# Kernel tuning notes

Measured on AMD Instinct MI355X. Metric: run time of the kernel, lower is better.

The kernel has to match this reference:

```python
import jax, jax.numpy as jnp
import numpy as np

N = 8192      # nodes
E = 131072    # global edges
SDIM = 256    # scalar channels
VDIM = 64     # vector channels
EDIM = 128    # edge feature dim
L = 5         # num_layers
DIN = 2 * SDIM + EDIM + 4        # [s_src, s_tgt, e, d, a, |p_src|, |p_tgt|]
DOUT = SDIM + 2 * VDIM + 1 + EDIM  # [m_s, w_v1, w_v2, w_p, e_new]
HID = SDIM


def setup_inputs() -> dict:
    key = jax.random.key(0)
    ks = jax.random.split(key, 12)
    s = jax.random.normal(ks[0], (N, SDIM), jnp.float32)
    v = 0.1 * jax.random.normal(ks[1], (N, 3, VDIM), jnp.float32)
    p = 3.0 * jax.random.normal(ks[2], (N, 3), jnp.float32)
    e = jax.random.normal(ks[3], (E, EDIM), jnp.float32)
    edge_index = jax.random.randint(ks[4], (2, E), 0, N, dtype=jnp.int32)
    W1 = jax.random.normal(ks[5], (L, DIN, HID), jnp.float32) / np.sqrt(DIN)
    W2 = jax.random.normal(ks[6], (L, HID, DOUT), jnp.float32) / np.sqrt(HID)
    U1 = jax.random.normal(ks[7], (L, SDIM, SDIM), jnp.float32) / np.sqrt(SDIM)
    U2 = jax.random.normal(ks[8], (L, SDIM, SDIM), jnp.float32) / np.sqrt(SDIM)
    return {
        's': s, 'v': v, 'p': p, 'e': e, 'edge_index': edge_index,
        'ln_g': jnp.ones((L, SDIM), jnp.float32),
        'ln_b': jnp.zeros((L, SDIM), jnp.float32),
        'W1': W1, 'b1': jnp.zeros((L, HID), jnp.float32),
        'W2': W2, 'b2': jnp.zeros((L, DOUT), jnp.float32),
        'U1': U1, 'bU1': jnp.zeros((L, SDIM), jnp.float32),
        'U2': U2, 'bU2': jnp.zeros((L, SDIM), jnp.float32),
    }


def _edge_attrs(edge_index, pos):
    # Faithful to calculate_edge_attrs (sqrt=True, no ligand-pocket branch)
    src, tgt = edge_index[0], edge_index[1]
    r = pos[tgt] - pos[src]                                   # [E,3]
    a = jnp.sum(pos[tgt] * pos[src], axis=-1)                 # [E]
    d = jnp.sqrt(jnp.clip(jnp.sum(r * r, axis=-1), 1e-6, None))
    r_norm = r / (1.0 + d[:, None])
    return d, a, r_norm


def reference(s, v, p, e, edge_index, ln_g, ln_b, W1, b1, W2, b2, U1, bU1, U2, bU2):
    src, tgt = edge_index[0], edge_index[1]
    d, a, rn = _edge_attrs(edge_index, p)
    # in-degree counts for 'mean' vector/position aggregation
    cnt = jnp.clip(jax.ops.segment_sum(jnp.ones((E,), s.dtype), tgt, num_segments=N), 1.0)
    for i in range(L):
        # LayerNorm on scalar channels (vectors passed through)
        mu = jnp.mean(s, axis=-1, keepdims=True)
        var = jnp.mean((s - mu) ** 2, axis=-1, keepdims=True)
        s_ln = ln_g[i] * (s - mu) * jax.lax.rsqrt(var + 1e-5) + ln_b[i]
        pn = jnp.linalg.norm(p, axis=-1, keepdims=True)       # use_pos_norm features
        # gather-compute edge messages
        feat = jnp.concatenate(
            [s_ln[src], s_ln[tgt], e, d[:, None], a[:, None], pn[src], pn[tgt]], axis=-1)
        h = jax.nn.silu(feat @ W1[i] + b1[i])                 # [E,HID]
        out = h @ W2[i] + b2[i]                               # [E,DOUT]
        m_s = out[:, :SDIM]
        wv1 = out[:, SDIM:SDIM + VDIM]
        wv2 = out[:, SDIM + VDIM:SDIM + 2 * VDIM]
        wp = out[:, SDIM + 2 * VDIM:SDIM + 2 * VDIM + 1]
        e_new = out[:, SDIM + 2 * VDIM + 1:]
        has_v = 0.0 if i == 0 else 1.0                        # has_v_in = (i > 0)
        m_v = has_v * wv1[:, None, :] * v[src] + wv2[:, None, :] * rn[:, :, None]  # [E,3,VDIM]
        m_p = jnp.tanh(wp) * rn                               # [E,3]
        # scatter-aggregate (sum for scalars, mean for vectors/positions)
        s = s + jax.ops.segment_sum(m_s, tgt, num_segments=N)
        v = v + jax.ops.segment_sum(m_v, tgt, num_segments=N) / cnt[:, None, None]
        p = p + jax.ops.segment_sum(m_p, tgt, num_segments=N) / cnt[:, None]
        if i < L - 1:                                         # use_mlp_update = (i < num_layers - 1)
            s = s + jax.nn.silu(s @ U1[i] + bU1[i]) @ U2[i] + bU2[i]
        e = jax.nn.silu(e_new)
        # recompute_edge_attributes=True: redo gather/distance math on new positions
        d, a, rn = _edge_attrs(edge_index, p)
    return s, v, e, p
```

## Files before the change

### kernel.cpp

```cpp
#include <hip/hip_runtime.h>
#include <hip/hip_bf16.h>

namespace {

constexpr int NN   = 8192;
constexpr int NE   = 131072;
constexpr int SD   = 256;
constexpr int ED   = 128;
constexpr int NL   = 5;
constexpr int DINc = 644;
constexpr int KE   = 160;
constexpr int TE   = 5;
constexpr int T2   = 8;
constexpr int DOUTc= 513;
constexpr int HIDc = 256;

typedef __bf16 bf16x8 __attribute__((ext_vector_type(8)));
typedef float  f32x4  __attribute__((ext_vector_type(4)));

__device__ __forceinline__ float siluf(float x) { return x / (1.0f + __expf(-x)); }

__device__ __forceinline__ void gl_lds16(const void* gsrc, void* lds_uniform_base) {
  __builtin_amdgcn_global_load_lds(
      (const __attribute__((address_space(1))) unsigned int*)gsrc,
      (__attribute__((address_space(3))) unsigned int*)lds_uniform_base, 16, 0, 0);
}

__device__ __forceinline__ void wait_vm4() {
  asm volatile("s_waitcnt vmcnt(4)" ::: "memory");
  __builtin_amdgcn_sched_barrier(0);
}
__device__ __forceinline__ void wait_vm0() {
  asm volatile("s_waitcnt vmcnt(0)" ::: "memory");
  __builtin_amdgcn_sched_barrier(0);
}

__device__ __host__ __forceinline__ int swz(int kc) { return (kc * 5) & 7; }
__device__ __forceinline__ int apos(int kc, int row) { return kc * 64  + (row ^ swz(kc)); }
__device__ __forceinline__ int bpos(int kc, int n)   { return kc * 256 + (n   ^ swz(kc)); }

enum { SRC_BF16 = 1 };

struct GemmArgs {
  const __hip_bfloat16* Wt;
  const float* bias;
  const __hip_bfloat16* Abf;
  __hip_bfloat16* bf_out;
  const __hip_bfloat16* Wtb;
  const float* biasb;
  __hip_bfloat16* bf_outb;
  int dual;
};

__device__ __forceinline__ uint4 cvt8f(const float* p) {
  alignas(16) __hip_bfloat16 t8[8];
#pragma unroll
  for (int i = 0; i < 8; i++) t8[i] = __float2bfloat16(p[i]);
  return *(const uint4*)t8;
}

template<int KTOT, int BM>
__global__ __launch_bounds__(256) void gemm_k(GemmArgs g) {
  constexpr int T = KTOT / 32;
  constexpr int NC = KTOT / 8;
  constexpr int RPT = 256 / BM;
  constexpr int RMASK = RPT - 1;
  __shared__ alignas(16) unsigned short Apan[NC * BM * 8];
  __shared__ alignas(16) unsigned short Bsh[2][4 * 256 * 8];
  const int tid = threadIdx.x, lane = tid & 63, wave = tid >> 6;
  const int l16 = lane & 15, lhi = lane >> 4;
  const __hip_bfloat16* wtp = g.Wt;
  const float* biasp = g.bias;
  __hip_bfloat16* outp = g.bf_out;
  int blk = blockIdx.x;
  {
    const int half = gridDim.x >> 1;
    if (g.dual && blk >= half) { blk -= half; wtp = g.Wtb; biasp = g.biasb; outp = g.bf_outb; }
  }
  const int row0 = blk * BM;
  const int ar = tid / RPT, aq = tid % RPT;
  const int arow = row0 + ar;
  f32x4 acc[BM / 16][4] = {};

  auto issueB = [&](int t, int buf) {
    const __hip_bfloat16* src = wtp + (size_t)t * 1024 * 8;
    unsigned short* dst = &Bsh[buf][0];
#pragma unroll
    for (int i = 0; i < 4; i++)
      gl_lds16(src + (size_t)(i * 256 + wave * 64 + lane) * 8, dst + (i * 256 + wave * 64) * 8);
  };

  issueB(0, 0);
#pragma unroll
  for (int j = 0; j < NC / RPT; j++) {
    const int c = j * RPT + aq;
    uint4 o = *(const uint4*)(g.Abf + (size_t)arow * KTOT + c * 8);
    *(uint4*)&Apan[(c * BM + (ar ^ swz(aq))) * 8] = o;
  }
  __syncthreads();

  int cur = 0;
  for (int t = 0; t < T; ++t) {
    if (t + 1 < T) { issueB(t + 1, cur ^ 1); wait_vm4(); }
    else           { wait_vm0(); }
    bf16x8 bfr[4];
#pragma unroll
    for (int f = 0; f < 4; f++)
      bfr[f] = *(const bf16x8*)&Bsh[cur][bpos(lhi, wave * 64 + f * 16 + l16) * 8];
#pragma unroll
    for (int fr = 0; fr < BM / 16; fr++) {
      const int kc = t * 4 + lhi;
      const bf16x8 afr = *(const bf16x8*)&Apan[(kc * BM + ((fr * 16 + l16) ^ swz(kc & RMASK))) * 8];
#pragma unroll
      for (int fc = 0; fc < 4; fc++)
        acc[fr][fc] = __builtin_amdgcn_mfma_f32_16x16x32_bf16(afr, bfr[fc], acc[fr][fc], 0, 0, 0);
    }
    cur ^= 1;
  }

#pragma unroll
  for (int fr = 0; fr < BM / 16; fr++) {
#pragma unroll
    for (int fc = 0; fc < 4; fc++) {
      const int n = wave * 64 + fc * 16 + l16;
#pragma unroll
      for (int r = 0; r < 4; r++) {
        const int row = row0 + fr * 16 + lhi * 4 + r;
        outp[(size_t)row * HIDc + n] = __float2bfloat16(acc[fr][fc][r] + biasp[n]);
      }
    }
  }
}

struct Node3Args {
  const __hip_bfloat16* W2a;
  const __hip_bfloat16* U1s;
  const __hip_bfloat16* U2s;
  const __hip_bfloat16* W1an;
  const __hip_bfloat16* W1bn;
  const float* b2L;
  const float* bU1;
  const float* bU2;
  const float* b1n;
  const float* lng;
  const float* lnb;
  const float* Hagg;
  const int* rawcnt;
  float* s_out;
  __hip_bfloat16* p1;
  __hip_bfloat16* p2;
};

template<int LAST>
__global__ __launch_bounds__(256) void node3_k(Node3Args g) {
  constexpr int BM = 32, RPT = 8, NC = 32, T = 8;
  __shared__ alignas(16) unsigned short Apan[NC * BM * 8];
  __shared__ alignas(16) unsigned short Bsh[2][4 * 256 * 8];
  __shared__ float red[2][4][32];
  const int tid = threadIdx.x, lane = tid & 63, wave = tid >> 6;
  const int l16 = lane & 15, lhi = lane >> 4;
  const int row0 = blockIdx.x * BM;
  const int ar = tid >> 3, aq = tid & 7;

  auto issueB = [&](const __hip_bfloat16* W, int t, int buf) {
    const __hip_bfloat16* src = W + (size_t)t * 1024 * 8;
    unsigned short* dst = &Bsh[buf][0];
#pragma unroll
    for (int i = 0; i < 4; i++)
      gl_lds16(src + (size_t)(i * 256 + wave * 64 + lane) * 8, dst + (i * 256 + wave * 64) * 8);
  };

  f32x4 acc[4][2];
  auto kloop = [&](const __hip_bfloat16* W) {
#pragma unroll
    for (int i = 0; i < 4; i++)
#pragma unroll
      for (int j = 0; j < 2; j++) acc[i][j] = f32x4{0.f, 0.f, 0.f, 0.f};
    int cur = 0;
    for (int t = 0; t < T; ++t) {
      if (t + 1 < T) { issueB(W, t + 1, cur ^ 1); wait_vm4(); }
      else           { wait_vm0(); }
      bf16x8 wfr[4], afr[2];
#pragma unroll
      for (int f = 0; f < 4; f++)
        wfr[f] = *(const bf16x8*)&Bsh[cur][bpos(lhi, wave * 64 + f * 16 + l16) * 8];
#pragma unroll
      for (int f = 0; f < 2; f++) {
        const int kc = t * 4 + lhi;
        afr[f] = *(const bf16x8*)&Apan[(kc * BM + ((f * 16 + l16) ^ swz(kc & 7))) * 8];
      }
#pragma unroll
      for (int fr = 0; fr < 4; fr++)
#pragma unroll
        for (int fc = 0; fc < 2; fc++)
          acc[fr][fc] = __builtin_amdgcn_mfma_f32_16x16x32_bf16(wfr[fr], afr[fc], acc[fr][fc], 0, 0, 0);
      cur ^= 1;
    }
  };

  issueB(g.W2a, 0, 0);
#pragma unroll
  for (int j = 0; j < NC / RPT; j++) {
    const int c = j * RPT + aq;
    uint4 o = cvt8f(g.Hagg + (size_t)(row0 + ar) * SD + c * 8);
    *(uint4*)&Apan[(c * BM + (ar ^ swz(aq))) * 8] = o;
  }
  __syncthreads();

  kloop(g.W2a);
  __syncthreads();
  if constexpr (!LAST) issueB(g.U1s, 0, 0);

#pragma unroll
  for (int fr = 0; fr < 4; fr++) {
    const int nb = wave * 64 + fr * 16 + lhi * 4;
    const int kc = nb >> 3, off = nb & 7;
    const f32x4 b4 = *(const f32x4*)(g.b2L + nb);
#pragma unroll
    for (int fc = 0; fc < 2; fc++) {
      const int row = fc * 16 + l16;
      const float rc = (float)g.rawcnt[row0 + row];
      float* sp = g.s_out + (size_t)(row0 + row) * SD + nb;
      f32x4 sold = *(const f32x4*)sp;
      alignas(8) __hip_bfloat16 hb[4];
      f32x4 s1;
#pragma unroll
      for (int r = 0; r < 4; r++) {
        s1[r] = sold[r] + acc[fr][fc][r] + rc * b4[r];
        hb[r] = __float2bfloat16(s1[r]);
      }
      *(f32x4*)sp = s1;
      if constexpr (!LAST)
        *(uint2*)&Apan[(kc * BM + (row ^ swz(kc & 7))) * 8 + off] = *(const uint2*)hb;
    }
  }
  if constexpr (LAST) return;

  __syncthreads();

  kloop(g.U1s);
  __syncthreads();
  issueB(g.U2s, 0, 0);
#pragma unroll
  for (int fr = 0; fr < 4; fr++) {
    const int nb = wave * 64 + fr * 16 + lhi * 4;
    const int kc = nb >> 3, off = nb & 7;
    const f32x4 b4 = *(const f32x4*)(g.bU1 + nb);
#pragma unroll
    for (int fc = 0; fc < 2; fc++) {
      const int row = fc * 16 + l16;
      alignas(8) __hip_bfloat16 hb[4];
#pragma unroll
      for (int r = 0; r < 4; r++)
        hb[r] = __float2bfloat16(siluf(acc[fr][fc][r] + b4[r]));
      *(uint2*)&Apan[(kc * BM + (row ^ swz(kc & 7))) * 8 + off] = *(const uint2*)hb;
    }
  }
  __syncthreads();

  kloop(g.U2s);
  float psum[2] = {0.f, 0.f}, psq[2] = {0.f, 0.f};
#pragma unroll
  for (int fr = 0; fr < 4; fr++) {
    const int nb = wave * 64 + fr * 16 + lhi * 4;
    const f32x4 b4 = *(const f32x4*)(g.bU2 + nb);
#pragma unroll
    for (int fc = 0; fc < 2; fc++) {
      const int row = fc * 16 + l16;
      float* sp = g.s_out + (size_t)(row0 + row) * SD + nb;
      f32x4 sv = *(const f32x4*)sp;
#pragma unroll
      for (int r = 0; r < 4; r++) {
        sv[r] += acc[fr][fc][r] + b4[r];
        psum[fc] += sv[r];
        psq[fc] += sv[r] * sv[r];
      }
      *(f32x4*)sp = sv;
      acc[fr][fc] = sv;
    }
  }
#pragma unroll
  for (int fc = 0; fc < 2; fc++) {
    psum[fc] += __shfl_xor(psum[fc], 16); psum[fc] += __shfl_xor(psum[fc], 32);
    psq[fc]  += __shfl_xor(psq[fc], 16);  psq[fc]  += __shfl_xor(psq[fc], 32);
  }
  if (lane < 16) {
    red[0][wave][lane] = psum[0]; red[0][wave][16 + lane] = psum[1];
    red[1][wave][lane] = psq[0];  red[1][wave][16 + lane] = psq[1];
  }
  __syncthreads();

  float mu2[2], rs2[2];
#pragma unroll
  for (int fc = 0; fc < 2; fc++) {
    const int ri = fc * 16 + l16;
    const float S = red[0][0][ri] + red[0][1][ri] + red[0][2][ri] + red[0][3][ri];
    const float Q = red[1][0][ri] + red[1][1][ri] + red[1][2][ri] + red[1][3][ri];
    const float mu = S * (1.0f / SD);
    const float var = Q * (1.0f / SD) - mu * mu;
    mu2[fc] = mu; rs2[fc] = rsqrtf(var + 1e-5f);
  }
#pragma unroll
  for (int fr = 0; fr < 4; fr++) {
    const int nb = wave * 64 + fr * 16 + lhi * 4;
    const int kc = nb >> 3, off = nb & 7;
    const f32x4 g4 = *(const f32x4*)(g.lng + nb);
    const f32x4 bb4 = *(const f32x4*)(g.lnb + nb);
#pragma unroll
    for (int fc = 0; fc < 2; fc++) {
      const int row = fc * 16 + l16;
      alignas(8) __hip_bfloat16 hb[4];
#pragma unroll
      for (int r = 0; r < 4; r++)
        hb[r] = __float2bfloat16(g4[r] * (acc[fr][fc][r] - mu2[fc]) * rs2[fc] + bb4[r]);
      *(uint2*)&Apan[(kc * BM + (row ^ swz(kc & 7))) * 8 + off] = *(const uint2*)hb;
    }
  }
  issueB(g.W1an, 0, 0);
  __syncthreads();

  kloop(g.W1an);
#pragma unroll
  for (int fr = 0; fr < 4; fr++) {
    const int nb = wave * 64 + fr * 16 + lhi * 4;
    const f32x4 b4 = *(const f32x4*)(g.b1n + nb);
#pragma unroll
    for (int fc = 0; fc < 2; fc++) {
      const int row = fc * 16 + l16;
      alignas(8) __hip_bfloat16 hb[4];
#pragma unroll
      for (int r = 0; r < 4; r++)
        hb[r] = __float2bfloat16(acc[fr][fc][r] + b4[r]);
      *(uint2*)(g.p1 + (size_t)(row0 + row) * SD + nb) = *(const uint2*)hb;
    }
  }
  issueB(g.W1bn, 0, 0);
  kloop(g.W1bn);
#pragma unroll
  for (int fr = 0; fr < 4; fr++) {
    const int nb = wave * 64 + fr * 16 + lhi * 4;
#pragma unroll
    for (int fc = 0; fc < 2; fc++) {
      const int row = fc * 16 + l16;
      alignas(8) __hip_bfloat16 hb[4];
#pragma unroll
      for (int r = 0; r < 4; r++)
        hb[r] = __float2bfloat16(acc[fr][fc][r]);
      *(uint2*)(g.p2 + (size_t)(row0 + row) * SD + nb) = *(const uint2*)hb;
    }
  }
}

struct FusedArgs {
  const __hip_bfloat16* W1e;
  const __hip_bfloat16* W2s;
  const float* b2L;
  const int* psrc;
  const int* ptgt;
  const int* iperm;
  const float* pos;
  const __hip_bfloat16* e_bf;
  const __hip_bfloat16* p1;
  const __hip_bfloat16* p2;
  const __hip_bfloat16* w384;
  float* rnp;
  float* mp;
  __hip_bfloat16* h_out;
  __hip_bfloat16* wv_out;
  __hip_bfloat16* e_bf_out;
  float* e_f32_out;
  int write_e_f32;
};

__global__ __launch_bounds__(256) void fused_k(FusedArgs g) {
  __shared__ alignas(16) unsigned short Ash[4 * 64 * 8];
  __shared__ alignas(16) unsigned short Bsh[2][4 * 256 * 8];
  __shared__ alignas(16) unsigned short Hsh[32 * 64 * 8];
  __shared__ float wps[4][64];
  __shared__ float RnL[64][3];
  __shared__ unsigned int EdL[64][2];
  __shared__ int Ei[64];
  const int tid = threadIdx.x, lane = tid & 63, wave = tid >> 6;
  const int l16 = lane & 15, lhi = lane >> 4;
  const int row0 = blockIdx.x * 64;
  const int ar = tid >> 2, aq = tid & 3;
  const int arow = row0 + ar;
  const int sn = g.psrc[arow], tn = g.ptgt[arow];

  auto issueW = [&](const __hip_bfloat16* W, int t, int buf) {
    const __hip_bfloat16* src = W + (size_t)t * 1024 * 8;
    unsigned short* dst = &Bsh[buf][0];
#pragma unroll
    for (int i = 0; i < 4; i++)
      gl_lds16(src + (size_t)(i * 256 + wave * 64 + lane) * 8, dst + (i * 256 + wave * 64) * 8);
  };
  auto loadA = [&](int t, uint4& o) {
    if (t < 4) {
      o = *(const uint4*)(g.e_bf + (size_t)arow * ED + t * 32 + aq * 8);
    } else {
      o.x = o.y = o.z = o.w = 0;
      if (aq == 0) { o.x = EdL[ar][0]; o.y = EdL[ar][1]; }
    }
  };

  uint4 a;
  loadA(0, a);
  issueW(g.W1e, 0, 0);

  if (tid < 64) {
    const int e = row0 + tid;
    Ei[tid] = g.iperm[e];
    const int s_ = g.psrc[e], t_ = g.ptgt[e];
    const float sx = g.pos[s_ * 3], sy = g.pos[s_ * 3 + 1], sz = g.pos[s_ * 3 + 2];
    const float tx = g.pos[t_ * 3], ty = g.pos[t_ * 3 + 1], tz = g.pos[t_ * 3 + 2];
    const float rx = tx - sx, ry = ty - sy, rz = tz - sz;
    const float av = tx * sx + ty * sy + tz * sz;
    const float rr = rx * rx + ry * ry + rz * rz;
    const float d = sqrtf(fmaxf(rr, 1e-6f));
    const float inv = 1.0f / (1.0f + d);
    const float r0 = rx * inv, r1 = ry * inv, r2 = rz * inv;
    RnL[tid][0] = r0; RnL[tid][1] = r1; RnL[tid][2] = r2;
    g.rnp[e * 3] = r0; g.rnp[e * 3 + 1] = r1; g.rnp[e * 3 + 2] = r2;
    alignas(8) __hip_bfloat16 q[4];
    q[0] = __float2bfloat16(d);
    q[1] = __float2bfloat16(av);
    q[2] = __float2bfloat16(sqrtf(sx * sx + sy * sy + sz * sz));
    q[3] = __float2bfloat16(sqrtf(tx * tx + ty * ty + tz * tz));
    EdL[tid][0] = ((const unsigned*)q)[0];
    EdL[tid][1] = ((const unsigned*)q)[1];
  }

#pragma unroll
  for (int j = 0; j < 8; j++) {
    const int c = j * 4 + aq;
    uint4 r1 = *(const uint4*)(g.p1 + (size_t)sn * SD + c * 8);
    uint4 r2 = *(const uint4*)(g.p2 + (size_t)tn * SD + c * 8);
    const __hip_bfloat16* h1 = (const __hip_bfloat16*)&r1;
    const __hip_bfloat16* h2 = (const __hip_bfloat16*)&r2;
    alignas(16) __hip_bfloat16 o8[8];
#pragma unroll
    for (int m = 0; m < 8; m++)
      o8[m] = __float2bfloat16(__bfloat162float(h1[m]) + __bfloat162float(h2[m]));
    *(uint4*)&Hsh[(c * 64 + (ar ^ swz(aq))) * 8] = *(const uint4*)o8;
  }

  f32x4 acc1[4][4] = {};
  int cur = 0;
  for (int t = 0; t < TE; ++t) {
    *(uint4*)&Ash[apos(aq, ar) * 8] = a;
    __syncthreads();
    if (t + 1 < TE) { issueW(g.W1e, t + 1, cur ^ 1); loadA(t + 1, a); }
    bf16x8 wfr[4], efr[4];
#pragma unroll
    for (int f = 0; f < 4; f++) {
      wfr[f] = *(const bf16x8*)&Bsh[cur][bpos(lhi, wave * 64 + f * 16 + l16) * 8];
      efr[f] = *(const bf16x8*)&Ash[apos(lhi, f * 16 + l16) * 8];
    }
#pragma unroll
    for (int fr = 0; fr < 4; fr++)
#pragma unroll
      for (int fc = 0; fc < 4; fc++)
        acc1[fr][fc] = __builtin_amdgcn_mfma_f32_16x16x32_bf16(wfr[fr], efr[fc], acc1[fr][fc], 0, 0, 0);
    __syncthreads();
    cur ^= 1;
  }

  issueW(g.W2s, 0, 0);

  float pw[4] = {0.f, 0.f, 0.f, 0.f};
#pragma unroll
  for (int fr = 0; fr < 4; fr++) {
    const int nb = wave * 64 + fr * 16 + lhi * 4;
    const int kc = nb >> 3, off = nb & 7;
    uint2 wr = *(const uint2*)(g.w384 + nb);
    const __hip_bfloat16* w4 = (const __hip_bfloat16*)&wr;
#pragma unroll
    for (int fc = 0; fc < 4; fc++) {
      const int row = fc * 16 + l16;
      unsigned short* slot = &Hsh[(kc * 64 + (row ^ swz(kc & 3))) * 8 + off];
      uint2 pr = *(const uint2*)slot;
      const __hip_bfloat16* pp = (const __hip_bfloat16*)&pr;
      alignas(8) __hip_bfloat16 hb[4];
#pragma unroll
      for (int r = 0; r < 4; r++) {
        const float hv = siluf(acc1[fr][fc][r] + __bfloat162float(pp[r]));
        hb[r] = __float2bfloat16(hv);
        pw[fc] += hv * __bfloat162float(w4[r]);
      }
      *(uint2*)slot = *(const uint2*)hb;
      *(uint2*)(g.h_out + (size_t)(row0 + row) * HIDc + nb) = *(const uint2*)hb;
    }
  }

#pragma unroll
  for (int fc = 0; fc < 4; fc++) {
    pw[fc] += __shfl_xor(pw[fc], 16);
    pw[fc] += __shfl_xor(pw[fc], 32);
  }
  if (lane < 16) {
#pragma unroll
    for (int fc = 0; fc < 4; fc++) wps[wave][fc * 16 + lane] = pw[fc];
  }
  __syncthreads();
  if (tid < 64) {
    const float s = wps[0][tid] + wps[1][tid] + wps[2][tid] + wps[3][tid];
    const float wpt = tanhf(s + g.b2L[384]);
    const int e = row0 + tid;
#pragma unroll
    for (int c = 0; c < 3; c++)
      g.mp[(size_t)e * 3 + c] = wpt * RnL[tid][c];
  }

  f32x4 acc2[4][4] = {};
  cur = 0;
  for (int t = 0; t < T2; ++t) {
    if (t + 1 < T2) { issueW(g.W2s, t + 1, cur ^ 1); wait_vm4(); }
    else            { wait_vm0(); }
    bf16x8 afr[4], bfr[4];
#pragma unroll
    for (int f = 0; f < 4; f++) {
      const int kc = t * 4 + lhi;
      afr[f] = *(const bf16x8*)&Hsh[(kc * 64 + ((f * 16 + l16) ^ swz(lhi))) * 8];
      bfr[f] = *(const bf16x8*)&Bsh[cur][bpos(lhi, wave * 64 + f * 16 + l16) * 8];
    }
#pragma unroll
    for (int fr = 0; fr < 4; fr++)
#pragma unroll
      for (int fc = 0; fc < 4; fc++)
        acc2[fr][fc] = __builtin_amdgcn_mfma_f32_16x16x32_bf16(afr[fr], bfr[fc], acc2[fr][fc], 0, 0, 0);
    cur ^= 1;
  }

#pragma unroll
  for (int fr = 0; fr < 4; fr++) {
#pragma unroll
    for (int fc = 0; fc < 4; fc++) {
      const int n = wave * 64 + fc * 16 + l16;
#pragma unroll
      for (int r = 0; r < 4; r++) {
        const int lr = fr * 16 + lhi * 4 + r;
        const int row = row0 + lr;
        const float valf = acc2[fr][fc][r];
        if (n < 128) {
          g.wv_out[(size_t)row * 128 + n] = __float2bfloat16(valf + g.b2L[256 + n]);
        } else {
          const float sv = siluf(valf + g.b2L[257 + n]);
          g.e_bf_out[(size_t)row * ED + (n - 128)] = __float2bfloat16(sv);
          if (g.write_e_f32) g.e_f32_out[(size_t)Ei[lr] * ED + (n - 128)] = sv;
        }
      }
    }
  }
}

__global__ __launch_bounds__(256) void ln_k(const float* __restrict__ s,
                                            const float* __restrict__ gl, const float* __restrict__ bl,
                                            __hip_bfloat16* __restrict__ s_ln) {
  const int wave = threadIdx.x >> 6, lane = threadIdx.x & 63;
  const int node = blockIdx.x * 4 + wave;
  const float* srow = s + (size_t)node * SD;
  float x[4], sum = 0.f, sq = 0.f;
#pragma unroll
  for (int i = 0; i < 4; i++) { x[i] = srow[lane * 4 + i]; sum += x[i]; sq += x[i] * x[i]; }
#pragma unroll
  for (int off = 1; off < 64; off <<= 1) { sum += __shfl_xor(sum, off); sq += __shfl_xor(sq, off); }
  const float mu = sum * (1.0f / SD);
  const float var = sq * (1.0f / SD) - mu * mu;
  const float rstd = rsqrtf(var + 1e-5f);
#pragma unroll
  for (int i = 0; i < 4; i++) {
    const int c = lane * 4 + i;
    s_ln[(size_t)node * SD + c] = __float2bfloat16(gl[c] * (x[i] - mu) * rstd + bl[c]);
  }
}

__global__ void cvt_e_k(const float* __restrict__ e, const int* __restrict__ iperm,
                        __hip_bfloat16* __restrict__ ebf) {
  const int idx = blockIdx.x * blockDim.x + threadIdx.x;
  const int pos = idx >> 4, c = idx & 15;
  const int src_e = iperm[pos];
  const float* p = e + (size_t)src_e * ED + c * 8;
  alignas(16) __hip_bfloat16 t8[8];
#pragma unroll
  for (int j = 0; j < 8; j++) t8[j] = __float2bfloat16(p[j]);
  *(uint4*)(ebf + (size_t)pos * ED + c * 8) = *(const uint4*)t8;
}

__global__ void count_k(const int* __restrict__ tgt, int* __restrict__ rawcnt) {
  const int e = blockIdx.x * blockDim.x + threadIdx.x;
  if (e < NE) atomicAdd(&rawcnt[tgt[e]], 1);
}

__global__ __launch_bounds__(256) void scan_k(const int* __restrict__ rawcnt, int* __restrict__ off) {
  __shared__ int ts[256];
  const int tid = threadIdx.x;
  const int base = tid * 32;
  int local[32];
  int s = 0;
#pragma unroll
  for (int i = 0; i < 32; i++) { local[i] = s; s += rawcnt[base + i]; }
  ts[tid] = s;
  __syncthreads();
  if (tid == 0) {
    int acc = 0;
    for (int i = 0; i < 256; i++) { int t = ts[i]; ts[i] = acc; acc += t; }
    off[NN] = acc;
  }
  __syncthreads();
  const int pre = ts[tid];
#pragma unroll
  for (int i = 0; i < 32; i++) off[base + i] = pre + local[i];
}

__global__ void scatter_k(const int* __restrict__ tgt, const int* __restrict__ srcp,
                          const int* __restrict__ off, int* __restrict__ cursor,
                          int* __restrict__ psrc, int* __restrict__ ptgt, int* __restrict__ iperm) {
  const int e = blockIdx.x * blockDim.x + threadIdx.x;
  if (e < NE) {
    const int t = tgt[e];
    const int pos = off[t] + atomicAdd(&cursor[t], 1);
    psrc[pos] = srcp[e];
    ptgt[pos] = t;
    iperm[pos] = e;
  }
}

__global__ __launch_bounds__(256) void agg_k(const int* __restrict__ off, const int* __restrict__ psrc,
                                             const __hip_bfloat16* __restrict__ h,
                                             const __hip_bfloat16* __restrict__ wv,
                                             const float* __restrict__ mp,
                                             const float* __restrict__ rnp,
                                             const float* __restrict__ v_old,
                                             const __hip_bfloat16* __restrict__ vbf_old,
                                             float* __restrict__ v_new,
                                             __hip_bfloat16* __restrict__ vbf_new,
                                             float* __restrict__ Hagg,
                                             float* __restrict__ p_o,
                                             int hasv) {
  const int n = blockIdx.x;
  const int c = threadIdx.x;
  const int e0 = off[n], e1 = off[n + 1];
  const int c3 = c >> 6, ln = c & 63;
  float hs = 0.f, vs = 0.f, ps = 0.f;
  int j = e0;
  for (; j + 2 <= e1; j += 2) {
    const float h0 = __bfloat162float(h[(size_t)j * HIDc + c]);
    const float h1 = __bfloat162float(h[(size_t)(j + 1) * HIDc + c]);
    hs += h0 + h1;
    if (c < 192) {
      const int s0 = psrc[j], s1 = psrc[j + 1];
      float m0 = __bfloat162float(wv[(size_t)j * 128 + 64 + ln]) * rnp[j * 3 + c3];
      float m1 = __bfloat162float(wv[(size_t)(j + 1) * 128 + 64 + ln]) * rnp[(j + 1) * 3 + c3];
      if (hasv) {
        m0 += __bfloat162float(wv[(size_t)j * 128 + ln]) * __bfloat162float(vbf_old[(size_t)s0 * 192 + c]);
        m1 += __bfloat162float(wv[(size_t)(j + 1) * 128 + ln]) * __bfloat162float(vbf_old[(size_t)s1 * 192 + c]);
      }
      vs += m0 + m1;
    } else if (c < 195) {
      ps += mp[j * 3 + (c - 192)] + mp[(j + 1) * 3 + (c - 192)];
    }
  }
  for (; j < e1; j++) {
    hs += __bfloat162float(h[(size_t)j * HIDc + c]);
    if (c < 192) {
      float mv = __bfloat162float(wv[(size_t)j * 128 + 64 + ln]) * rnp[j * 3 + c3];
      if (hasv) mv += __bfloat162float(wv[(size_t)j * 128 + ln]) * __bfloat162float(vbf_old[(size_t)psrc[j] * 192 + c]);
      vs += mv;
    } else if (c < 195) {
      ps += mp[j * 3 + (c - 192)];
    }
  }
  Hagg[(size_t)n * HIDc + c] = hs;
  const float inv = 1.0f / fmaxf((float)(e1 - e0), 1.0f);
  if (c < 192) {
    const float nv = v_old[(size_t)n * 192 + c] + vs * inv;
    v_new[(size_t)n * 192 + c] = nv;
    vbf_new[(size_t)n * 192 + c] = __float2bfloat16(nv);
  } else if (c < 195) {
    p_o[n * 3 + (c - 192)] += ps * inv;
  }
}

__global__ void zero_k(float* __restrict__ ptr, int n) {
  const int i = blockIdx.x * blockDim.x + threadIdx.x;
  if (i < n) ptr[i] = 0.f;
}

__global__ void prep_w1abs_k(const float* __restrict__ W1, __hip_bfloat16* __restrict__ W1aS,
                             __hip_bfloat16* __restrict__ W1bS) {
  const int idx = blockIdx.x * blockDim.x + threadIdx.x;
  if (idx >= NL * T2 * 1024) return;
  const int p = idx & 1023, t = (idx >> 10) % T2, l = idx / (T2 * 1024);
  const int kc = p >> 8, n = (p & 255) ^ swz(kc);
  alignas(16) __hip_bfloat16 a8[8], b8[8];
#pragma unroll
  for (int j = 0; j < 8; j++) {
    const int k = t * 32 + kc * 8 + j;
    a8[j] = __float2bfloat16(W1[((size_t)l * DINc + k) * HIDc + n]);
    b8[j] = __float2bfloat16(W1[((size_t)l * DINc + 256 + k) * HIDc + n]);
  }
  *(uint4*)(W1aS + (size_t)idx * 8) = *(const uint4*)a8;
  *(uint4*)(W1bS + (size_t)idx * 8) = *(const uint4*)b8;
}

__global__ void prep_w1es_k(const float* __restrict__ W1, __hip_bfloat16* __restrict__ W1eS) {
  const int idx = blockIdx.x * blockDim.x + threadIdx.x;
  if (idx >= NL * TE * 1024) return;
  const int p = idx & 1023, t = (idx >> 10) % TE, l = idx / (TE * 1024);
  const int kc = p >> 8, n = (p & 255) ^ swz(kc);
  alignas(16) __hip_bfloat16 e8[8];
#pragma unroll
  for (int j = 0; j < 8; j++) {
    const int k = t * 32 + kc * 8 + j;
    const int row = (k < 128) ? (512 + k) : ((k < 132) ? (640 + (k - 128)) : -1);
    e8[j] = __float2bfloat16(row >= 0 ? W1[((size_t)l * DINc + row) * HIDc + n] : 0.f);
  }
  *(uint4*)(W1eS + (size_t)idx * 8) = *(const uint4*)e8;
}

__global__ void prep_w2s_k(const float* __restrict__ W2, __hip_bfloat16* __restrict__ W2sS,
                           __hip_bfloat16* __restrict__ W2aS) {
  const int idx = blockIdx.x * blockDim.x + threadIdx.x;
  if (idx >= NL * T2 * 1024) return;
  const int p = idx & 1023, t = (idx >> 10) & 7, l = idx >> 13;
  const int kc = p >> 8, n = (p & 255) ^ swz(kc);
  const float* W2l = W2 + (size_t)l * HIDc * DOUTc;
  const int cs = (n < 128) ? (256 + n) : (257 + n);
  alignas(16) __hip_bfloat16 s8[8], a8[8];
#pragma unroll
  for (int j = 0; j < 8; j++) {
    const int k = t * 32 + kc * 8 + j;
    s8[j] = __float2bfloat16(W2l[(size_t)k * DOUTc + cs]);
    a8[j] = __float2bfloat16(W2l[(size_t)k * DOUTc + n]);
  }
  *(uint4*)(W2sS + (size_t)idx * 8) = *(const uint4*)s8;
  *(uint4*)(W2aS + (size_t)idx * 8) = *(const uint4*)a8;
}

__global__ void prep_uts_k(const float* __restrict__ U1, const float* __restrict__ U2,
                           __hip_bfloat16* __restrict__ U1S, __hip_bfloat16* __restrict__ U2S) {
  const int idx = blockIdx.x * blockDim.x + threadIdx.x;
  if (idx >= NL * T2 * 1024) return;
  const int p = idx & 1023, t = (idx >> 10) & 7, l = idx >> 13;
  const int kc = p >> 8, n = (p & 255) ^ swz(kc);
  alignas(16) __hip_bfloat16 u1[8], u2[8];
#pragma unroll
  for (int j = 0; j < 8; j++) {
    const int k = t * 32 + kc * 8 + j;
    u1[j] = __float2bfloat16(U1[((size_t)l * HIDc + k) * HIDc + n]);
    u2[j] = __float2bfloat16(U2[((size_t)l * HIDc + k) * HIDc + n]);
  }
  *(uint4*)(U1S + (size_t)idx * 8) = *(const uint4*)u1;
  *(uint4*)(U2S + (size_t)idx * 8) = *(const uint4*)u2;
}

__global__ void prep_w384_k(const float* __restrict__ W2, __hip_bfloat16* __restrict__ w384) {
  const int idx = blockIdx.x * blockDim.x + threadIdx.x;
  if (idx >= NL * HIDc) return;
  const int k = idx & 255, l = idx >> 8;
  w384[idx] = __float2bfloat16(W2[((size_t)l * HIDc + k) * DOUTc + 384]);
}

}

extern "C" void kernel_launch(void* const* d_in, const int* in_sizes, int n_in,
                              void* d_out, int out_size, void* d_ws, size_t ws_size,
                              hipStream_t stream) {
  (void)in_sizes; (void)n_in; (void)out_size; (void)ws_size;
  const float* s_in = (const float*)d_in[0];
  const float* v_in = (const float*)d_in[1];
  const float* p_in = (const float*)d_in[2];
  const float* e_in = (const float*)d_in[3];
  const int*   ei   = (const int*)d_in[4];
  const float* ln_g = (const float*)d_in[5];
  const float* ln_b = (const float*)d_in[6];
  const float* W1   = (const float*)d_in[7];
  const float* b1   = (const float*)d_in[8];
  const float* W2   = (const float*)d_in[9];
  const float* b2   = (const float*)d_in[10];
  const float* U1   = (const float*)d_in[11];
  const float* bU1  = (const float*)d_in[12];
  const float* U2   = (const float*)d_in[13];
  const float* bU2  = (const float*)d_in[14];

  float* s_o = (float*)d_out;
  float* v_o = s_o + (size_t)NN * SD;
  float* e_o = v_o + (size_t)NN * 192;
  float* p_o = e_o + (size_t)NE * ED;

  const int* srcp = ei;
  const int* tgtp = ei + NE;

  char* wp = (char*)d_ws;
  auto alloc = [&](size_t bytes) -> char* {
    char* r = wp; wp += (bytes + 255) & ~(size_t)255; return r;
  };
  __hip_bfloat16* s_ln = (__hip_bfloat16*)alloc((size_t)NN * SD * 2);
  __hip_bfloat16* hbuf = (__hip_bfloat16*)alloc((size_t)NE * HIDc * 2);
  __hip_bfloat16* ebf  = (__hip_bfloat16*)alloc((size_t)NE * ED * 2);
  __hip_bfloat16* wvbuf= (__hip_bfloat16*)alloc((size_t)NE * 128 * 2);
  __hip_bfloat16* p1buf= (__hip_bfloat16*)alloc((size_t)NN * SD * 2);
  __hip_bfloat16* p2buf= (__hip_bfloat16*)alloc((size_t)NN * SD * 2);
  __hip_bfloat16* vbf0 = (__hip_bfloat16*)alloc((size_t)NN * 192 * 2);
  __hip_bfloat16* vbf1 = (__hip_bfloat16*)alloc((size_t)NN * 192 * 2);
  float* rnpbuf= (float*)alloc((size_t)NE * 3 * 4);
  float* Hagg  = (float*)alloc((size_t)NN * SD * 4);
  float* vprev = (float*)alloc((size_t)NN * 192 * 4);
  float* mpbuf = (float*)alloc((size_t)NE * 3 * 4);
  float* zerobias = (float*)alloc(256 * 4);
  int*   rawcnt= (int*)alloc((size_t)NN * 4);
  int*   offb  = (int*)alloc((size_t)(NN + 1) * 4);
  int*   cursor= (int*)alloc((size_t)NN * 4);
  int*   psrcb = (int*)alloc((size_t)NE * 4);
  int*   ptgtb = (int*)alloc((size_t)NE * 4);
  int*   ipermb= (int*)alloc((size_t)NE * 4);
  __hip_bfloat16* W1aS = (__hip_bfloat16*)alloc((size_t)NL * T2 * 1024 * 8 * 2);
  __hip_bfloat16* W1bS = (__hip_bfloat16*)alloc((size_t)NL * T2 * 1024 * 8 * 2);
  __hip_bfloat16* W1eS = (__hip_bfloat16*)alloc((size_t)NL * TE * 1024 * 8 * 2);
  __hip_bfloat16* W2sS = (__hip_bfloat16*)alloc((size_t)NL * T2 * 1024 * 8 * 2);
  __hip_bfloat16* W2aS = (__hip_bfloat16*)alloc((size_t)NL * T2 * 1024 * 8 * 2);
  __hip_bfloat16* U1S  = (__hip_bfloat16*)alloc((size_t)NL * T2 * 1024 * 8 * 2);
  __hip_bfloat16* U2S  = (__hip_bfloat16*)alloc((size_t)NL * T2 * 1024 * 8 * 2);
  __hip_bfloat16* w384 = (__hip_bfloat16*)alloc((size_t)NL * HIDc * 2);

  hipMemcpyAsync(s_o, s_in, (size_t)NN * SD * 4, hipMemcpyDeviceToDevice, stream);
  hipMemcpyAsync(vprev, v_in, (size_t)NN * 192 * 4, hipMemcpyDeviceToDevice, stream);
  hipMemcpyAsync(p_o, p_in, (size_t)NN * 3 * 4, hipMemcpyDeviceToDevice, stream);

  prep_w1abs_k<<<(NL * T2 * 1024 + 255) / 256, 256, 0, stream>>>(W1, W1aS, W1bS);
  prep_w1es_k<<<(NL * TE * 1024 + 255) / 256, 256, 0, stream>>>(W1, W1eS);
  prep_w2s_k<<<(NL * T2 * 1024 + 255) / 256, 256, 0, stream>>>(W2, W2sS, W2aS);
  prep_uts_k<<<(NL * T2 * 1024 + 255) / 256, 256, 0, stream>>>(U1, U2, U1S, U2S);
  prep_w384_k<<<(NL * HIDc + 255) / 256, 256, 0, stream>>>(W2, w384);
  zero_k<<<1, 256, 0, stream>>>(zerobias, 256);

  zero_k<<<(NN + 255) / 256, 256, 0, stream>>>((float*)rawcnt, NN);
  zero_k<<<(NN + 255) / 256, 256, 0, stream>>>((float*)cursor, NN);
  count_k<<<NE / 256, 256, 0, stream>>>(tgtp, rawcnt);
  scan_k<<<1, 256, 0, stream>>>(rawcnt, offb);
  scatter_k<<<NE / 256, 256, 0, stream>>>(tgtp, srcp, offb, cursor, psrcb, ptgtb, ipermb);
  cvt_e_k<<<NE * 16 / 256, 256, 0, stream>>>(e_in, ipermb, ebf);

  ln_k<<<NN / 4, 256, 0, stream>>>(s_o, ln_g, ln_b, s_ln);
  GemmArgs gp{};
  gp.Wt = W1aS; gp.bias = b1; gp.bf_out = p1buf;
  gp.Wtb = W1bS; gp.biasb = zerobias; gp.bf_outb = p2buf;
  gp.Abf = s_ln; gp.dual = 1;
  gemm_k<256, 64><<<2 * NN / 64, 256, 0, stream>>>(gp);

  for (int l = 0; l < NL; l++) {
    FusedArgs gf{};
    gf.W1e = W1eS + (size_t)l * TE * 1024 * 8;
    gf.W2s = W2sS + (size_t)l * T2 * 1024 * 8;
    gf.b2L = b2 + l * DOUTc;
    gf.psrc = psrcb; gf.ptgt = ptgtb; gf.iperm = ipermb;
    gf.pos = p_o; gf.e_bf = ebf;
    gf.p1 = p1buf; gf.p2 = p2buf; gf.w384 = w384 + l * HIDc;
    gf.rnp = rnpbuf; gf.mp = mpbuf;
    gf.h_out = hbuf; gf.wv_out = wvbuf; gf.e_bf_out = ebf; gf.e_f32_out = e_o;
    gf.write_e_f32 = (l == NL - 1) ? 1 : 0;
    fused_k<<<NE / 64, 256, 0, stream>>>(gf);

    const float* vold = (l & 1) ? (const float*)v_o : (const float*)vprev;
    float* vnew = (l & 1) ? vprev : v_o;
    const __hip_bfloat16* vbold = (l & 1) ? (const __hip_bfloat16*)vbf1 : (const __hip_bfloat16*)vbf0;
    __hip_bfloat16* vbnew = (l & 1) ? vbf0 : vbf1;
    agg_k<<<NN, 256, 0, stream>>>(offb, psrcb, hbuf, wvbuf, mpbuf, rnpbuf,
                                  vold, vbold, vnew, vbnew, Hagg, p_o, (l > 0) ? 1 : 0);

    Node3Args gn{};
    gn.W2a = W2aS + (size_t)l * T2 * 1024 * 8;
    gn.U1s = U1S + (size_t)l * T2 * 1024 * 8;
    gn.U2s = U2S + (size_t)l * T2 * 1024 * 8;
    gn.b2L = b2 + l * DOUTc; gn.bU1 = bU1 + l * HIDc; gn.bU2 = bU2 + l * HIDc;
    gn.Hagg = Hagg; gn.rawcnt = rawcnt; gn.s_out = s_o;
    if (l < NL - 1) {
      gn.W1an = W1aS + (size_t)(l + 1) * T2 * 1024 * 8;
      gn.W1bn = W1bS + (size_t)(l + 1) * T2 * 1024 * 8;
      gn.b1n = b1 + (l + 1) * HIDc;
      gn.lng = ln_g + (l + 1) * SD; gn.lnb = ln_b + (l + 1) * SD;
      gn.p1 = p1buf; gn.p2 = p2buf;
      node3_k<0><<<NN / 32, 256, 0, stream>>>(gn);
    } else {
      node3_k<1><<<NN / 32, 256, 0, stream>>>(gn);
    }
  }
}
```

Baseline: 0.9998 ms.

## Fuse hidden-activation segment sum into edge kernel via atomics, drop h buffer

```diff
diff --git a/kernel.cpp b/kernel.cpp
--- a/kernel.cpp
+++ b/kernel.cpp
@@ -144,7 +144,7 @@
   const float* b1n;
   const float* lng;
   const float* lnb;
-  const float* Hagg;
+  float* Hagg;
   const int* rawcnt;
   float* s_out;
   __hip_bfloat16* p1;
@@ -199,11 +199,15 @@
   };
 
   issueB(g.W2a, 0, 0);
+  const f32x4 z4 = {0.f, 0.f, 0.f, 0.f};
 #pragma unroll
   for (int j = 0; j < NC / RPT; j++) {
     const int c = j * RPT + aq;
-    uint4 o = cvt8f(g.Hagg + (size_t)(row0 + ar) * SD + c * 8);
+    float* hp = g.Hagg + (size_t)(row0 + ar) * SD + c * 8;
+    uint4 o = cvt8f(hp);
     *(uint4*)&Apan[(c * BM + (ar ^ swz(aq))) * 8] = o;
+    *(f32x4*)hp = z4;
+    *(f32x4*)(hp + 4) = z4;
   }
   __syncthreads();
 
@@ -365,7 +369,7 @@
   const __hip_bfloat16* w384;
   float* rnp;
   float* mp;
-  __hip_bfloat16* h_out;
+  float* HaggA;
   __hip_bfloat16* wv_out;
   __hip_bfloat16* e_bf_out;
   float* e_f32_out;
@@ -379,6 +383,7 @@
   __shared__ float wps[4][64];
   __shared__ float RnL[64][3];
   __shared__ unsigned int EdL[64][2];
+  __shared__ int TgL[64];
   __shared__ int Ei[64];
   const int tid = threadIdx.x, lane = tid & 63, wave = tid >> 6;
   const int l16 = lane & 15, lhi = lane >> 4;
@@ -411,6 +416,7 @@
     const int e = row0 + tid;
     Ei[tid] = g.iperm[e];
     const int s_ = g.psrc[e], t_ = g.ptgt[e];
+    TgL[tid] = t_;
     const float sx = g.pos[s_ * 3], sy = g.pos[s_ * 3 + 1], sz = g.pos[s_ * 3 + 2];
     const float tx = g.pos[t_ * 3], ty = g.pos[t_ * 3 + 1], tz = g.pos[t_ * 3 + 2];
     const float rx = tx - sx, ry = ty - sy, rz = tz - sz;
@@ -488,7 +494,6 @@
         pw[fc] += hv * __bfloat162float(w4[r]);
       }
       *(uint2*)slot = *(const uint2*)hb;
-      *(uint2*)(g.h_out + (size_t)(row0 + row) * HIDc + nb) = *(const uint2*)hb;
     }
   }
 
@@ -551,6 +556,22 @@
       }
     }
   }
+
+  {
+    const int c = tid;
+    const int kc = c >> 3, off = c & 7;
+    float seg = 0.f;
+    int curn = TgL[0];
+    for (int row = 0; row < 64; ++row) {
+      const int nid = TgL[row];
+      if (nid != curn) {
+        atomicAdd(&g.HaggA[(size_t)curn * HIDc + c], seg);
+        seg = 0.f; curn = nid;
+      }
+      seg += __bfloat162float(*(const __hip_bfloat16*)&Hsh[(kc * 64 + (row ^ swz(kc & 3))) * 8 + off]);
+    }
+    atomicAdd(&g.HaggA[(size_t)curn * HIDc + c], seg);
+  }
 }
 
 __global__ __launch_bounds__(256) void ln_k(const float* __restrict__ s,
@@ -626,7 +647,6 @@
 }
 
 __global__ __launch_bounds__(256) void agg_k(const int* __restrict__ off, const int* __restrict__ psrc,
-                                             const __hip_bfloat16* __restrict__ h,
                                              const __hip_bfloat16* __restrict__ wv,
                                              const float* __restrict__ mp,
                                              const float* __restrict__ rnp,
@@ -634,19 +654,15 @@
                                              const __hip_bfloat16* __restrict__ vbf_old,
                                              float* __restrict__ v_new,
                                              __hip_bfloat16* __restrict__ vbf_new,
-                                             float* __restrict__ Hagg,
                                              float* __restrict__ p_o,
                                              int hasv) {
   const int n = blockIdx.x;
   const int c = threadIdx.x;
   const int e0 = off[n], e1 = off[n + 1];
   const int c3 = c >> 6, ln = c & 63;
-  float hs = 0.f, vs = 0.f, ps = 0.f;
+  float vs = 0.f, ps = 0.f;
   int j = e0;
   for (; j + 2 <= e1; j += 2) {
-    const float h0 = __bfloat162float(h[(size_t)j * HIDc + c]);
-    const float h1 = __bfloat162float(h[(size_t)(j + 1) * HIDc + c]);
-    hs += h0 + h1;
     if (c < 192) {
       const int s0 = psrc[j], s1 = psrc[j + 1];
       float m0 = __bfloat162float(wv[(size_t)j * 128 + 64 + ln]) * rnp[j * 3 + c3];
@@ -661,7 +677,6 @@
     }
   }
   for (; j < e1; j++) {
-    hs += __bfloat162float(h[(size_t)j * HIDc + c]);
     if (c < 192) {
       float mv = __bfloat162float(wv[(size_t)j * 128 + 64 + ln]) * rnp[j * 3 + c3];
       if (hasv) mv += __bfloat162float(wv[(size_t)j * 128 + ln]) * __bfloat162float(vbf_old[(size_t)psrc[j] * 192 + c]);
@@ -670,7 +685,6 @@
       ps += mp[j * 3 + (c - 192)];
     }
   }
-  Hagg[(size_t)n * HIDc + c] = hs;
   const float inv = 1.0f / fmaxf((float)(e1 - e0), 1.0f);
   if (c < 192) {
     const float nv = v_old[(size_t)n * 192 + c] + vs * inv;
@@ -796,7 +810,6 @@
     char* r = wp; wp += (bytes + 255) & ~(size_t)255; return r;
   };
   __hip_bfloat16* s_ln = (__hip_bfloat16*)alloc((size_t)NN * SD * 2);
-  __hip_bfloat16* hbuf = (__hip_bfloat16*)alloc((size_t)NE * HIDc * 2);
   __hip_bfloat16* ebf  = (__hip_bfloat16*)alloc((size_t)NE * ED * 2);
   __hip_bfloat16* wvbuf= (__hip_bfloat16*)alloc((size_t)NE * 128 * 2);
   __hip_bfloat16* p1buf= (__hip_bfloat16*)alloc((size_t)NN * SD * 2);
@@ -833,6 +846,7 @@
   prep_uts_k<<<(NL * T2 * 1024 + 255) / 256, 256, 0, stream>>>(U1, U2, U1S, U2S);
   prep_w384_k<<<(NL * HIDc + 255) / 256, 256, 0, stream>>>(W2, w384);
   zero_k<<<1, 256, 0, stream>>>(zerobias, 256);
+  zero_k<<<(NN * SD + 255) / 256, 256, 0, stream>>>(Hagg, NN * SD);
 
   zero_k<<<(NN + 255) / 256, 256, 0, stream>>>((float*)rawcnt, NN);
   zero_k<<<(NN + 255) / 256, 256, 0, stream>>>((float*)cursor, NN);
@@ -856,8 +870,8 @@
     gf.psrc = psrcb; gf.ptgt = ptgtb; gf.iperm = ipermb;
     gf.pos = p_o; gf.e_bf = ebf;
     gf.p1 = p1buf; gf.p2 = p2buf; gf.w384 = w384 + l * HIDc;
-    gf.rnp = rnpbuf; gf.mp = mpbuf;
-    gf.h_out = hbuf; gf.wv_out = wvbuf; gf.e_bf_out = ebf; gf.e_f32_out = e_o;
+    gf.rnp = rnpbuf; gf.mp = mpbuf; gf.HaggA = Hagg;
+    gf.wv_out = wvbuf; gf.e_bf_out = ebf; gf.e_f32_out = e_o;
     gf.write_e_f32 = (l == NL - 1) ? 1 : 0;
     fused_k<<<NE / 64, 256, 0, stream>>>(gf);
 
@@ -865,8 +879,8 @@
     float* vnew = (l & 1) ? vprev : v_o;
     const __hip_bfloat16* vbold = (l & 1) ? (const __hip_bfloat16*)vbf1 : (const __hip_bfloat16*)vbf0;
     __hip_bfloat16* vbnew = (l & 1) ? vbf0 : vbf1;
-    agg_k<<<NN, 256, 0, stream>>>(offb, psrcb, hbuf, wvbuf, mpbuf, rnpbuf,
-                                  vold, vbold, vnew, vbnew, Hagg, p_o, (l > 0) ? 1 : 0);
+    agg_k<<<NN, 256, 0, stream>>>(offb, psrcb, wvbuf, mpbuf, rnpbuf,
+                                  vold, vbold, vnew, vbnew, p_o, (l > 0) ? 1 : 0);
 
     Node3Args gn{};
     gn.W2a = W2aS + (size_t)l * T2 * 1024 * 8;
```

Result: slower. 1.065 ms (+6.5%).
